# Optimization experiments

Measured on AMD Instinct MI355X. Metric: run time of the kernel, lower is better.

## Reference

```python
import jax, jax.numpy as jnp
import numpy as np

B, D, U = 8192, 128, 128  # batch, input_dim, units (D == U required by the tile/reshape sign path)
CLIP = 20.0
EPS = 1e-7


def setup_inputs() -> dict:
    key = jax.random.key(0)
    ks = jax.random.split(key, 6)
    x = jax.random.normal(ks[0], (B, D), dtype=jnp.float32)
    # initializers: w ~ N(1, 0.1), m ~ N(-1, 0.1), g ~ N(0, 0.1)
    w_hat = 1.0 + 0.1 * jax.random.normal(ks[1], (D, U), dtype=jnp.float32)
    m_hat = -1.0 + 0.1 * jax.random.normal(ks[2], (D, U), dtype=jnp.float32)
    w_hat_prime = 1.0 + 0.1 * jax.random.normal(ks[3], (D, U), dtype=jnp.float32)
    m_hat_prime = -1.0 + 0.1 * jax.random.normal(ks[4], (D, U), dtype=jnp.float32)
    g = 0.1 * jax.random.normal(ks[5], (U,), dtype=jnp.float32)
    return {"x": x, "w_hat": w_hat, "m_hat": m_hat,
            "w_hat_prime": w_hat_prime, "m_hat_prime": m_hat_prime, "g": g}


def reference(x, w_hat, m_hat, w_hat_prime, m_hat_prime, g):
    w1 = jnp.tanh(w_hat) * jax.nn.sigmoid(m_hat)            # [D, U]
    w2 = jnp.tanh(w_hat_prime) * jax.nn.sigmoid(m_hat_prime)  # [D, U]
    a1 = x @ w1                                              # additive path [B, U]
    # multiplicative (log-space) path
    m1 = jnp.exp(jnp.minimum(jnp.log(jnp.maximum(jnp.abs(x), EPS)) @ w2, CLIP))
    # sign-correction path: faithful to tf concat/reshape layout
    w1s = jnp.abs(w2).reshape(-1)                            # [D*U], row-major over (D, U)
    xs = jnp.tile(x, (1, U))                                 # [B, U*D]
    sgn = jnp.sign(xs) * w1s + (1.0 - w1s)                   # [B, D*U]
    ms = jnp.prod(sgn.reshape(-1, U, D), axis=2)             # [B, U]
    g1 = jax.nn.sigmoid(g)                                   # [U]
    return g1 * a1 + (1.0 - g1) * m1 * jnp.clip(ms, -1.0, 1.0)
```

## Files before the change

kernel.cpp:

```cpp
#include <hip/hip_runtime.h>
#include <cmath>


typedef __bf16  bf16x8 __attribute__((ext_vector_type(8)));
typedef float   f32x4  __attribute__((ext_vector_type(4)));

#define NROWS 8192
#define KDIM  128
#define UDIM  128

__device__ __forceinline__ unsigned short f2bf(float f) {
    union { float f; unsigned int u; } v; v.f = f;
    unsigned int u = v.u;
    unsigned int r = (u + 0x7FFFu + ((u >> 16) & 1u)) >> 16;
    return (unsigned short)r;
}

__device__ __forceinline__ unsigned int pck(unsigned short a, unsigned short b) {
    return (unsigned int)a | ((unsigned int)b << 16);
}

__device__ __forceinline__ float sigmoidf_(float v) {
    return 1.0f / (1.0f + expf(-v));
}

__global__ void nalu_prep(const float* __restrict__ w_hat,
                          const float* __restrict__ m_hat,
                          const float* __restrict__ whp,
                          const float* __restrict__ mhp,
                          unsigned short* __restrict__ Bsw) {
    int i = blockIdx.x * 256 + threadIdx.x;
    int n = i >> 7;
    int k = i & 127;
    int dk = k * 128 + n;
    int ud = n * 128 + k;

    float w1v = tanhf(w_hat[dk]) * sigmoidf_(m_hat[dk]);
    float w2v = tanhf(whp[dk])   * sigmoidf_(mhp[dk]);
    float a   = fabsf(tanhf(whp[ud]) * sigmoidf_(mhp[ud]));
    float f   = 1.0f - 2.0f * a;
    float Sv  = fmaxf(logf(fmaxf(fabsf(f), 1e-38f)), -80.0f);
    float ngv = (f < 0.0f) ? 1.0f : 0.0f;

    int nblk = n >> 4, l16 = n & 15, kstep = k >> 5, quad = (k >> 3) & 3, j = k & 7;
    int lane = quad * 16 + l16;
    int base = ((nblk * 4 + kstep) * 64 + lane) * 8 + j;
    const int MATSTRIDE = 8 * 4 * 64 * 8;

    Bsw[base]                 = f2bf(w1v);
    Bsw[base + MATSTRIDE]     = f2bf(w2v);
    Bsw[base + 2 * MATSTRIDE] = f2bf(Sv);
    Bsw[base + 3 * MATSTRIDE] = f2bf(ngv);
}

__global__ __launch_bounds__(256, 1)
void nalu_main(const float* __restrict__ x,
               const unsigned short* __restrict__ Bsw,
               const float* __restrict__ g,
               float* __restrict__ out) {
    __shared__ __align__(16) unsigned short As[3][32][136];

    const int t    = threadIdx.x;
    const int wave = t >> 6;
    const int lane = t & 63;
    const int quad = lane >> 4;
    const int l16  = lane & 15;
    const int rowblk = blockIdx.x * 32;

    bf16x8 Bf[4][2][4];
    const bf16x8* Bp = reinterpret_cast<const bf16x8*>(Bsw);
    #pragma unroll
    for (int mat = 0; mat < 4; ++mat)
        #pragma unroll
        for (int ns = 0; ns < 2; ++ns)
            #pragma unroll
            for (int ks = 0; ks < 4; ++ks) {
                int nblk = wave * 2 + ns;
                Bf[mat][ns][ks] = Bp[((mat * 8 + nblk) * 4 + ks) * 64 + lane];
            }

    const float4* xv = reinterpret_cast<const float4*>(x + rowblk * 128);
    #pragma unroll
    for (int it = 0; it < 4; ++it) {
        int idx  = t + it * 256;
        int row  = idx >> 5;
        int col4 = idx & 31;
        float4 v = xv[idx];
        float vv[4] = {v.x, v.y, v.z, v.w};
        unsigned short sx[4], sl[4], sn[4];
        #pragma unroll
        for (int j = 0; j < 4; ++j) {
            float f = vv[j];
            sx[j] = f2bf(f);
            sl[j] = f2bf(logf(fmaxf(fabsf(f), 1e-7f)));
            sn[j] = (f < 0.0f) ? 0x3F80u : 0u;
        }
        uint2 px = {pck(sx[0], sx[1]), pck(sx[2], sx[3])};
        uint2 pl = {pck(sl[0], sl[1]), pck(sl[2], sl[3])};
        uint2 pn = {pck(sn[0], sn[1]), pck(sn[2], sn[3])};
        *reinterpret_cast<uint2*>(&As[0][row][col4 * 4]) = px;
        *reinterpret_cast<uint2*>(&As[1][row][col4 * 4]) = pl;
        *reinterpret_cast<uint2*>(&As[2][row][col4 * 4]) = pn;
    }
    __syncthreads();

    f32x4 accA[2][2], accM[2][2], accS[2][2], accC[2][2];
    #pragma unroll
    for (int ms = 0; ms < 2; ++ms)
        #pragma unroll
        for (int ns = 0; ns < 2; ++ns) {
            f32x4 z = {0.0f, 0.0f, 0.0f, 0.0f};
            accA[ms][ns] = z; accM[ms][ns] = z; accS[ms][ns] = z; accC[ms][ns] = z;
        }

    #pragma unroll
    for (int ks = 0; ks < 4; ++ks) {
        bf16x8 Ax[2], Al[2], An[2];
        #pragma unroll
        for (int ms = 0; ms < 2; ++ms) {
            int m = ms * 16 + l16;
            int k = ks * 32 + quad * 8;
            Ax[ms] = *reinterpret_cast<const bf16x8*>(&As[0][m][k]);
            Al[ms] = *reinterpret_cast<const bf16x8*>(&As[1][m][k]);
            An[ms] = *reinterpret_cast<const bf16x8*>(&As[2][m][k]);
        }
        #pragma unroll
        for (int ms = 0; ms < 2; ++ms)
            #pragma unroll
            for (int ns = 0; ns < 2; ++ns) {
                accA[ms][ns] = __builtin_amdgcn_mfma_f32_16x16x32_bf16(Ax[ms], Bf[0][ns][ks], accA[ms][ns], 0, 0, 0);
                accM[ms][ns] = __builtin_amdgcn_mfma_f32_16x16x32_bf16(Al[ms], Bf[1][ns][ks], accM[ms][ns], 0, 0, 0);
                accS[ms][ns] = __builtin_amdgcn_mfma_f32_16x16x32_bf16(An[ms], Bf[2][ns][ks], accS[ms][ns], 0, 0, 0);
                accC[ms][ns] = __builtin_amdgcn_mfma_f32_16x16x32_bf16(An[ms], Bf[3][ns][ks], accC[ms][ns], 0, 0, 0);
            }
    }

    #pragma unroll
    for (int ns = 0; ns < 2; ++ns) {
        int u = wave * 32 + ns * 16 + l16;
        float g1 = sigmoidf_(g[u]);
        float om = 1.0f - g1;
        #pragma unroll
        for (int ms = 0; ms < 2; ++ms) {
            int rbase = rowblk + ms * 16 + quad * 4;
            #pragma unroll
            for (int r = 0; r < 4; ++r) {
                float a1 = accA[ms][ns][r];
                float ml = accM[ms][ns][r];
                float sl = accS[ms][ns][r];
                float cn = accC[ms][ns][r];
                float par = 1.0f - 2.0f * (cn - 2.0f * floorf(cn * 0.5f));
                float mterm = par * expf(fminf(ml, 20.0f) + sl);
                out[(rbase + r) * 128 + u] = g1 * a1 + om * mterm;
            }
        }
    }
}

extern "C" void kernel_launch(void* const* d_in, const int* in_sizes, int n_in,
                              void* d_out, int out_size, void* d_ws, size_t ws_size,
                              hipStream_t stream) {
    const float* x     = (const float*)d_in[0];
    const float* w_hat = (const float*)d_in[1];
    const float* m_hat = (const float*)d_in[2];
    const float* whp   = (const float*)d_in[3];
    const float* mhp   = (const float*)d_in[4];
    const float* g     = (const float*)d_in[5];
    unsigned short* Bsw = (unsigned short*)d_ws;
    float* outp = (float*)d_out;

    nalu_prep<<<64, 256, 0, stream>>>(w_hat, m_hat, whp, mhp, Bsw);
    nalu_main<<<256, 256, 0, stream>>>(x, Bsw, g, outp);
}
```

Before: 70.64 us.

## Halve row tile, raise occupancy, stream B fragments per k-step, use fast intrinsics

The main kernel now processes 16 rows per block instead of 32 and launches 512 blocks with launch bounds allowing 3 blocks per CU. The B fragments are no longer preloaded in full into registers; they are double-buffered per k-step from global memory. Fast __expf/__logf intrinsics replace the libm calls. The goal is more parallelism and lower register pressure so global latency is hidden across 256 CUs. The cost is twice as many B fragment loads in total and slightly less accurate transcendentals.

```diff
diff --git a/kernel.cpp b/kernel.cpp
--- a/kernel.cpp
+++ b/kernel.cpp
@@ -4,10 +4,6 @@
 
 typedef __bf16  bf16x8 __attribute__((ext_vector_type(8)));
 typedef float   f32x4  __attribute__((ext_vector_type(4)));
-
-#define NROWS 8192
-#define KDIM  128
-#define UDIM  128
 
 __device__ __forceinline__ unsigned short f2bf(float f) {
     union { float f; unsigned int u; } v; v.f = f;
@@ -21,7 +17,7 @@
 }
 
 __device__ __forceinline__ float sigmoidf_(float v) {
-    return 1.0f / (1.0f + expf(-v));
+    return 1.0f / (1.0f + __expf(-v));
 }
 
 __global__ void nalu_prep(const float* __restrict__ w_hat,
@@ -39,7 +35,7 @@
     float w2v = tanhf(whp[dk])   * sigmoidf_(mhp[dk]);
     float a   = fabsf(tanhf(whp[ud]) * sigmoidf_(mhp[ud]));
     float f   = 1.0f - 2.0f * a;
-    float Sv  = fmaxf(logf(fmaxf(fabsf(f), 1e-38f)), -80.0f);
+    float Sv  = fmaxf(__logf(fmaxf(fabsf(f), 1e-38f)), -80.0f);
     float ngv = (f < 0.0f) ? 1.0f : 0.0f;
 
     int nblk = n >> 4, l16 = n & 15, kstep = k >> 5, quad = (k >> 3) & 3, j = k & 7;
@@ -53,35 +49,25 @@
     Bsw[base + 3 * MATSTRIDE] = f2bf(ngv);
 }
 
-__global__ __launch_bounds__(256, 1)
+__global__ __launch_bounds__(256, 3)
 void nalu_main(const float* __restrict__ x,
                const unsigned short* __restrict__ Bsw,
                const float* __restrict__ g,
                float* __restrict__ out) {
-    __shared__ __align__(16) unsigned short As[3][32][136];
+    __shared__ __align__(16) unsigned short As[3][16][136];
 
     const int t    = threadIdx.x;
     const int wave = t >> 6;
     const int lane = t & 63;
     const int quad = lane >> 4;
     const int l16  = lane & 15;
-    const int rowblk = blockIdx.x * 32;
+    const int rowblk = blockIdx.x * 16;
 
-    bf16x8 Bf[4][2][4];
     const bf16x8* Bp = reinterpret_cast<const bf16x8*>(Bsw);
-    #pragma unroll
-    for (int mat = 0; mat < 4; ++mat)
-        #pragma unroll
-        for (int ns = 0; ns < 2; ++ns)
-            #pragma unroll
-            for (int ks = 0; ks < 4; ++ks) {
-                int nblk = wave * 2 + ns;
-                Bf[mat][ns][ks] = Bp[((mat * 8 + nblk) * 4 + ks) * 64 + lane];
-            }
 
     const float4* xv = reinterpret_cast<const float4*>(x + rowblk * 128);
     #pragma unroll
-    for (int it = 0; it < 4; ++it) {
+    for (int it = 0; it < 2; ++it) {
         int idx  = t + it * 256;
         int row  = idx >> 5;
         int col4 = idx & 31;
@@ -92,7 +78,7 @@
         for (int j = 0; j < 4; ++j) {
             float f = vv[j];
             sx[j] = f2bf(f);
-            sl[j] = f2bf(logf(fmaxf(fabsf(f), 1e-7f)));
+            sl[j] = f2bf(__logf(fmaxf(fabsf(f), 1e-7f)));
             sn[j] = (f < 0.0f) ? 0x3F80u : 0u;
         }
         uint2 px = {pck(sx[0], sx[1]), pck(sx[2], sx[3])};
@@ -102,37 +88,51 @@
         *reinterpret_cast<uint2*>(&As[1][row][col4 * 4]) = pl;
         *reinterpret_cast<uint2*>(&As[2][row][col4 * 4]) = pn;
     }
+
+    f32x4 accA[2], accM[2], accS[2], accC[2];
+    #pragma unroll
+    for (int ns = 0; ns < 2; ++ns) {
+        f32x4 z = {0.0f, 0.0f, 0.0f, 0.0f};
+        accA[ns] = z; accM[ns] = z; accS[ns] = z; accC[ns] = z;
+    }
+
+    bf16x8 Bcur[4][2], Bnxt[4][2];
+    #pragma unroll
+    for (int mat = 0; mat < 4; ++mat)
+        #pragma unroll
+        for (int ns = 0; ns < 2; ++ns)
+            Bcur[mat][ns] = Bp[((mat * 8 + wave * 2 + ns) * 4 + 0) * 64 + lane];
+
     __syncthreads();
-
-    f32x4 accA[2][2], accM[2][2], accS[2][2], accC[2][2];
-    #pragma unroll
-    for (int ms = 0; ms < 2; ++ms)
-        #pragma unroll
-        for (int ns = 0; ns < 2; ++ns) {
-            f32x4 z = {0.0f, 0.0f, 0.0f, 0.0f};
-            accA[ms][ns] = z; accM[ms][ns] = z; accS[ms][ns] = z; accC[ms][ns] = z;
-        }
 
     #pragma unroll
     for (int ks = 0; ks < 4; ++ks) {
-        bf16x8 Ax[2], Al[2], An[2];
+        if (ks < 3) {
+            #pragma unroll
+            for (int mat = 0; mat < 4; ++mat)
+                #pragma unroll
+                for (int ns = 0; ns < 2; ++ns)
+                    Bnxt[mat][ns] = Bp[((mat * 8 + wave * 2 + ns) * 4 + (ks + 1)) * 64 + lane];
+        }
+        int m = l16;
+        int k = ks * 32 + quad * 8;
+        bf16x8 Ax = *reinterpret_cast<const bf16x8*>(&As[0][m][k]);
+        bf16x8 Al = *reinterpret_cast<const bf16x8*>(&As[1][m][k]);
+        bf16x8 An = *reinterpret_cast<const bf16x8*>(&As[2][m][k]);
         #pragma unroll
-        for (int ms = 0; ms < 2; ++ms) {
-            int m = ms * 16 + l16;
-            int k = ks * 32 + quad * 8;
-            Ax[ms] = *reinterpret_cast<const bf16x8*>(&As[0][m][k]);
-            Al[ms] = *reinterpret_cast<const bf16x8*>(&As[1][m][k]);
-            An[ms] = *reinterpret_cast<const bf16x8*>(&As[2][m][k]);
+        for (int ns = 0; ns < 2; ++ns) {
+            accA[ns] = __builtin_amdgcn_mfma_f32_16x16x32_bf16(Ax, Bcur[0][ns], accA[ns], 0, 0, 0);
+            accM[ns] = __builtin_amdgcn_mfma_f32_16x16x32_bf16(Al, Bcur[1][ns], accM[ns], 0, 0, 0);
+            accS[ns] = __builtin_amdgcn_mfma_f32_16x16x32_bf16(An, Bcur[2][ns], accS[ns], 0, 0, 0);
+            accC[ns] = __builtin_amdgcn_mfma_f32_16x16x32_bf16(An, Bcur[3][ns], accC[ns], 0, 0, 0);
         }
-        #pragma unroll
-        for (int ms = 0; ms < 2; ++ms)
+        if (ks < 3) {
             #pragma unroll
-            for (int ns = 0; ns < 2; ++ns) {
-                accA[ms][ns] = __builtin_amdgcn_mfma_f32_16x16x32_bf16(Ax[ms], Bf[0][ns][ks], accA[ms][ns], 0, 0, 0);
-                accM[ms][ns] = __builtin_amdgcn_mfma_f32_16x16x32_bf16(Al[ms], Bf[1][ns][ks], accM[ms][ns], 0, 0, 0);
-                accS[ms][ns] = __builtin_amdgcn_mfma_f32_16x16x32_bf16(An[ms], Bf[2][ns][ks], accS[ms][ns], 0, 0, 0);
-                accC[ms][ns] = __builtin_amdgcn_mfma_f32_16x16x32_bf16(An[ms], Bf[3][ns][ks], accC[ms][ns], 0, 0, 0);
-            }
+            for (int mat = 0; mat < 4; ++mat)
+                #pragma unroll
+                for (int ns = 0; ns < 2; ++ns)
+                    Bcur[mat][ns] = Bnxt[mat][ns];
+        }
     }
 
     #pragma unroll
@@ -140,19 +140,16 @@
         int u = wave * 32 + ns * 16 + l16;
         float g1 = sigmoidf_(g[u]);
         float om = 1.0f - g1;
+        int rbase = rowblk + quad * 4;
         #pragma unroll
-        for (int ms = 0; ms < 2; ++ms) {
-            int rbase = rowblk + ms * 16 + quad * 4;
-            #pragma unroll
-            for (int r = 0; r < 4; ++r) {
-                float a1 = accA[ms][ns][r];
-                float ml = accM[ms][ns][r];
-                float sl = accS[ms][ns][r];
-                float cn = accC[ms][ns][r];
-                float par = 1.0f - 2.0f * (cn - 2.0f * floorf(cn * 0.5f));
-                float mterm = par * expf(fminf(ml, 20.0f) + sl);
-                out[(rbase + r) * 128 + u] = g1 * a1 + om * mterm;
-            }
+        for (int r = 0; r < 4; ++r) {
+            float a1 = accA[ns][r];
+            float ml = accM[ns][r];
+            float sl = accS[ns][r];
+            float cn = accC[ns][r];
+            float par = 1.0f - 2.0f * (cn - 2.0f * floorf(cn * 0.5f));
+            float mterm = par * __expf(fminf(ml, 20.0f) + sl);
+            out[(rbase + r) * 128 + u] = g1 * a1 + om * mterm;
         }
     }
 }
@@ -170,5 +167,5 @@
     float* outp = (float*)d_out;
 
     nalu_prep<<<64, 256, 0, stream>>>(w_hat, m_hat, whp, mhp, Bsw);
-    nalu_main<<<256, 256, 0, stream>>>(x, Bsw, g, outp);
+    nalu_main<<<512, 256, 0, stream>>>(x, Bsw, g, outp);
 }
```

Result: slower. 73.39 us (+3.9%).
